# Performance work log

Measured on AMD Instinct MI355X. Metric: run time of the kernel, lower is better.

## Reference

```python
import jax, jax.numpy as jnp
import numpy as np

VOCAB, HDIM, NC = 32000, 256, 5
B, L = 256, 512  # L must be a power of 2 (complete binary tree, depth log2(L))


def setup_inputs() -> dict:
    key = jax.random.key(0)
    ks = jax.random.split(key, 8)
    s_e = 1.0 / np.sqrt(HDIM)
    s_r = 1.0 / np.sqrt(2 * HDIM)
    return {
        "tokens": jax.random.randint(ks[0], (B, L), 0, VOCAB),                        # leaf word ids
        "embed_table": jax.random.normal(ks[1], (VOCAB, HDIM), jnp.float32),          # nn.Embedding
        "WR_w": jax.random.uniform(ks[2], (HDIM, 2 * HDIM), jnp.float32, -s_r, s_r),  # Linear(2H->H)
        "WR_b": jax.random.uniform(ks[3], (HDIM,), jnp.float32, -s_r, s_r),
        "WF_w": jax.random.uniform(ks[4], (HDIM, HDIM), jnp.float32, -s_e, s_e),      # Linear(H->H)
        "WF_b": jax.random.uniform(ks[5], (HDIM,), jnp.float32, -s_e, s_e),
        "WO_w": jax.random.uniform(ks[6], (NC, HDIM), jnp.float32, -s_e, s_e),        # Linear(H->NC)
        "WO_b": jax.random.uniform(ks[7], (NC,), jnp.float32, -s_e, s_e),
    }


def reference(tokens, embed_table, WR_w, WR_b, WF_w, WF_b, WO_w, WO_b):
    # Leaves: embedding gather. [B, L, H]
    e = embed_table[tokens]
    # Batched-by-depth tree composition: tanh(WR(cat(left, right))) per level.
    # Loop is over log2(L) levels (static), fully vectorized within each level.
    while e.shape[1] > 1:
        cat = jnp.concatenate([e[:, 0::2], e[:, 1::2]], axis=-1)   # [B, n/2, 2H]
        e = jnp.tanh(jnp.einsum('bnd,hd->bnh', cat, WR_w) + WR_b)  # [B, n/2, H]
    root = e[:, 0]  # [B, H]
    # classify: WO(ReLU(WF(root)))
    hidden = jax.nn.relu(root @ WF_w.T + WF_b)
    return hidden @ WO_w.T + WO_b  # [B, NC] logits
```

## Files before the change

kernel.cpp:

```cpp
#include <hip/hip_runtime.h>
#include <hip/hip_bf16.h>

typedef __bf16 bf16_t;
typedef __bf16 bf16x8 __attribute__((ext_vector_type(8)));
typedef __bf16 bf16x4 __attribute__((ext_vector_type(4)));
typedef float f32x4 __attribute__((ext_vector_type(4)));

__device__ __forceinline__ bf16_t f2bf(float f) {
    __hip_bfloat16 h = __float2bfloat16(f);
    return __builtin_bit_cast(bf16_t, h);
}

__device__ __forceinline__ float tanh_fast(float s) {
    float e2x = __expf(2.0f * s);
    return 1.0f - 2.0f * __builtin_amdgcn_rcpf(e2x + 1.0f);
}

__device__ __forceinline__ int swz(int u) { return u ^ ((u >> 3) & 7); }
__device__ __forceinline__ int actswz(int a) {
    return a ^ ((((a >> 10) ^ (a >> 13)) & 7) << 4);
}

#define GLD16(g, l)                                                        \
    __builtin_amdgcn_global_load_lds(                                      \
        (const __attribute__((address_space(1))) void*)(g),                \
        (__attribute__((address_space(3))) void*)(l), 16, 0, 0)

#define WAITV3() asm volatile("s_waitcnt vmcnt(3)" ::: "memory")
#define WAITV2() asm volatile("s_waitcnt vmcnt(2)" ::: "memory")
#define WAITV0() asm volatile("s_waitcnt vmcnt(0)" ::: "memory")
#define BAR() __builtin_amdgcn_s_barrier()

__global__ void __launch_bounds__(256) setup_kernel(const float* __restrict__ table,
                                                    const float* __restrict__ WRw,
                                                    const float* __restrict__ WFw,
                                                    bf16_t* __restrict__ tableBf,
                                                    bf16_t* __restrict__ Wbf,
                                                    bf16_t* __restrict__ Wfrag,
                                                    float* __restrict__ WFwT) {
    const int b = blockIdx.x, tid = threadIdx.x;
    if (b < 8000) {
        int i = b * 256 + tid;
        float4 v = ((const float4*)table)[i];
        bf16x4 o;
        o[0] = f2bf(v.x); o[1] = f2bf(v.y); o[2] = f2bf(v.z); o[3] = f2bf(v.w);
        ((bf16x4*)tableBf)[i] = o;
    } else if (b < 8128) {
        int i = (b - 8000) * 256 + tid;
        float4 v = ((const float4*)WRw)[i];
        bf16x4 o;
        o[0] = f2bf(v.x); o[1] = f2bf(v.y); o[2] = f2bf(v.z); o[3] = f2bf(v.w);
        ((bf16x4*)Wbf)[i] = o;
    } else if (b < 8192) {
        int gt = (b - 8128) * 256 + tid;
        int n16 = gt >> 10, rem = gt & 1023;
        int kt = rem >> 6, ln = rem & 63;
        int r = n16 * 16 + (ln & 15);
        int c = kt * 32 + (ln >> 4) * 8;
        const float4* s = (const float4*)(WRw + (long)r * 512 + c);
        float4 v0 = s[0], v1 = s[1];
        bf16x8 o;
        o[0] = f2bf(v0.x); o[1] = f2bf(v0.y); o[2] = f2bf(v0.z); o[3] = f2bf(v0.w);
        o[4] = f2bf(v1.x); o[5] = f2bf(v1.y); o[6] = f2bf(v1.z); o[7] = f2bf(v1.w);
        *(bf16x8*)(Wfrag + (size_t)gt * 8) = o;
    } else {
        int i0 = (b - 8192) * 1024 + tid * 4;
        float4 v;
        v.x = WFw[((i0 + 0) & 255) * 256 + ((i0 + 0) >> 8)];
        v.y = WFw[((i0 + 1) & 255) * 256 + ((i0 + 1) >> 8)];
        v.z = WFw[((i0 + 2) & 255) * 256 + ((i0 + 2) >> 8)];
        v.w = WFw[((i0 + 3) & 255) * 256 + ((i0 + 3) >> 8)];
        *(float4*)(WFwT + i0) = v;
    }
}

__global__ void __launch_bounds__(512) l1_kernel(const int* __restrict__ tokens,
                                                 const bf16_t* __restrict__ tableBf,
                                                 const bf16_t* __restrict__ W,
                                                 const float* __restrict__ bias,
                                                 bf16_t* __restrict__ out) {
    __shared__ __align__(16) char lds[73728];
    const int tid = threadIdx.x, lane = tid & 63, w = tid >> 6;
    const int wm = w >> 2, wn = w & 3, lr = lane & 15, g = lane >> 4;
    const long brow = (long)blockIdx.x * 128;

    const int ua = (w << 6) + swz(lane);
    const int arow = ua >> 2, acolE = (ua & 3) << 3;
    const long m = brow + arow;
    const int tokA = tokens[2 * m], tokB = tokens[2 * m + 1];
    const bf16_t* paLo = tableBf + (long)tokA * 256 + acolE;
    const bf16_t* paHi = tableBf + (long)tokB * 256 + acolE;

    const int ub0 = (w << 6) + swz(lane);
    const int ub1 = ((w + 8) << 6) + swz(lane);
    const bf16_t* pb0 = W + (long)(ub0 >> 2) * 512 + ((ub0 & 3) << 3);
    const bf16_t* pb1 = W + (long)(ub1 >> 2) * 512 + ((ub1 & 3) << 3);

    float bv[4];
#pragma unroll
    for (int nt = 0; nt < 4; ++nt) bv[nt] = bias[(wn << 6) + (nt << 4) + lr];

    int offA[4], offB[4];
#pragma unroll
    for (int mt = 0; mt < 4; ++mt)
        offA[mt] = swz((((wm << 6) + (mt << 4) + lr) << 2) + g) << 4;
#pragma unroll
    for (int nt = 0; nt < 4; ++nt)
        offB[nt] = 8192 + (swz((((wn << 6) + (nt << 4) + lr) << 2) + g) << 4);

    auto stage = [&](int s, int kt) {
        char* base = lds + s * 24576;
        bool lo = kt < 256;
        GLD16((lo ? paLo : paHi) + (kt & 255), base + (w << 10));
        GLD16(pb0 + kt, base + 8192 + (w << 10));
        GLD16(pb1 + kt, base + 8192 + ((w + 8) << 10));
    };

    f32x4 acc[4][4];
    const f32x4 zero = {0.f, 0.f, 0.f, 0.f};
#pragma unroll
    for (int i = 0; i < 4; ++i)
#pragma unroll
        for (int j = 0; j < 4; ++j) acc[i][j] = zero;

    stage(0, 0);
    stage(1, 32);
    WAITV3(); BAR();

#pragma unroll
    for (int t = 0; t < 16; ++t) {
        const char* base = lds + (t % 3) * 24576;
        if (t + 2 < 16) stage((t + 2) % 3, (t + 2) << 5);
        bf16x8 af[4], bfr[4];
#pragma unroll
        for (int mt = 0; mt < 4; ++mt) af[mt] = *(const bf16x8*)(base + offA[mt]);
#pragma unroll
        for (int nt = 0; nt < 4; ++nt) bfr[nt] = *(const bf16x8*)(base + offB[nt]);
#pragma unroll
        for (int mt = 0; mt < 4; ++mt)
#pragma unroll
            for (int nt = 0; nt < 4; ++nt)
                acc[mt][nt] = __builtin_amdgcn_mfma_f32_16x16x32_bf16(
                    af[mt], bfr[nt], acc[mt][nt], 0, 0, 0);
        if (t < 14)      { WAITV3(); BAR(); }
        else if (t == 14){ WAITV0(); BAR(); }
    }

    const int crow = g << 2;
#pragma unroll
    for (int nt = 0; nt < 4; ++nt) {
        int col = (wn << 6) + (nt << 4) + lr;
#pragma unroll
        for (int mt = 0; mt < 4; ++mt) {
            long row0 = brow + (wm << 6) + (mt << 4) + crow;
#pragma unroll
            for (int r = 0; r < 4; ++r)
                out[(row0 + r) * 256 + col] = f2bf(tanh_fast(acc[mt][nt][r] + bv[nt]));
        }
    }
}

__global__ void __launch_bounds__(512) tree_kernel(const bf16_t* __restrict__ l1out,
                                                   const bf16_t* __restrict__ W,
                                                   const bf16_t* __restrict__ Wfrag,
                                                   const float* __restrict__ bias,
                                                   const float* __restrict__ WFwT,
                                                   const float* __restrict__ WFb,
                                                   const float* __restrict__ WOw,
                                                   const float* __restrict__ WOb,
                                                   float* __restrict__ out) {
    __shared__ __align__(16) char stg[73728];
    __shared__ __align__(16) char act[65536];
    __shared__ float hid[256];

    const int tid = threadIdx.x, lane = tid & 63, w = tid >> 6;
    const int wm = w >> 2, wn = w & 3, lr = lane & 15, g = lane >> 4;
    const int crow = g << 2;
    const bf16_t* Abase = l1out + (size_t)blockIdx.x * 65536;

    const int ua = (w << 6) + swz(lane);
    const bf16_t* pa = Abase + (long)(ua >> 2) * 512 + ((ua & 3) << 3);
    const int ub0 = (w << 6) + swz(lane);
    const int ub1 = ((w + 8) << 6) + swz(lane);
    const bf16_t* pb0 = W + (long)(ub0 >> 2) * 512 + ((ub0 & 3) << 3);
    const bf16_t* pb1 = W + (long)(ub1 >> 2) * 512 + ((ub1 & 3) << 3);

    float bv[4];
#pragma unroll
    for (int nt = 0; nt < 4; ++nt) bv[nt] = bias[(wn << 6) + (nt << 4) + lr];
    float bvT[2];
#pragma unroll
    for (int nt = 0; nt < 2; ++nt) bvT[nt] = bias[(w << 5) + (nt << 4) + lr];

    int offB[4];
#pragma unroll
    for (int nt = 0; nt < 4; ++nt)
        offB[nt] = swz((((wn << 6) + (nt << 4) + lr) << 2) + g) << 4;

    {
        int offA[4];
#pragma unroll
        for (int mt = 0; mt < 4; ++mt)
            offA[mt] = swz((((wm << 6) + (mt << 4) + lr) << 2) + g) << 4;

        auto stage = [&](int s, int kt) {
            char* base = stg + s * 24576;
            GLD16(pa + kt, base + (w << 10));
            GLD16(pb0 + kt, base + 8192 + (w << 10));
            GLD16(pb1 + kt, base + 8192 + ((w + 8) << 10));
        };

        f32x4 acc[4][4];
        const f32x4 zero = {0.f, 0.f, 0.f, 0.f};
#pragma unroll
        for (int i = 0; i < 4; ++i)
#pragma unroll
            for (int j = 0; j < 4; ++j) acc[i][j] = zero;

        stage(0, 0); stage(1, 32);
        WAITV3(); BAR();
#pragma unroll
        for (int t = 0; t < 16; ++t) {
            const char* base = stg + (t % 3) * 24576;
            if (t + 2 < 16) stage((t + 2) % 3, (t + 2) << 5);
            bf16x8 af[4], bfr[4];
#pragma unroll
            for (int mt = 0; mt < 4; ++mt) af[mt] = *(const bf16x8*)(base + 8192 * 0 + offA[mt]);
#pragma unroll
            for (int nt = 0; nt < 4; ++nt) bfr[nt] = *(const bf16x8*)(base + 8192 + offB[nt]);
#pragma unroll
            for (int mt = 0; mt < 4; ++mt)
#pragma unroll
                for (int nt = 0; nt < 4; ++nt)
                    acc[mt][nt] = __builtin_amdgcn_mfma_f32_16x16x32_bf16(
                        af[mt], bfr[nt], acc[mt][nt], 0, 0, 0);
            if (t < 14)      { WAITV3(); BAR(); }
            else if (t == 14){ WAITV0(); BAR(); }
        }
#pragma unroll
        for (int nt = 0; nt < 4; ++nt) {
            int col = (wn << 6) + (nt << 4) + lr;
#pragma unroll
            for (int mt = 0; mt < 4; ++mt) {
                int m0 = (wm << 6) + (mt << 4) + crow;
#pragma unroll
                for (int r = 0; r < 4; ++r) {
                    int a = ((m0 + r) << 9) + (col << 1);
                    *(bf16_t*)(act + actswz(a)) = f2bf(tanh_fast(acc[mt][nt][r] + bv[nt]));
                }
            }
        }
        __syncthreads();
    }

    {
        auto stageB = [&](int s, int kt) {
            char* base = stg + s * 16384;
            GLD16(pb0 + kt, base + (w << 10));
            GLD16(pb1 + kt, base + ((w + 8) << 10));
        };
        f32x4 acc[2][4];
        const f32x4 zero = {0.f, 0.f, 0.f, 0.f};
#pragma unroll
        for (int i = 0; i < 2; ++i)
#pragma unroll
            for (int j = 0; j < 4; ++j) acc[i][j] = zero;

        stageB(0, 0); stageB(1, 32);
        WAITV2(); BAR();
#pragma unroll
        for (int t = 0; t < 16; ++t) {
            const char* base = stg + (t % 3) * 16384;
            if (t + 2 < 16) stageB((t + 2) % 3, (t + 2) << 5);
            bf16x8 af[2], bfr[4];
#pragma unroll
            for (int mt = 0; mt < 2; ++mt) {
                int row = (wm << 5) + (mt << 4) + lr;
                int a = (row << 10) + (t << 6) + (g << 4);
                af[mt] = *(const bf16x8*)(act + actswz(a));
            }
#pragma unroll
            for (int nt = 0; nt < 4; ++nt) bfr[nt] = *(const bf16x8*)(base + offB[nt]);
#pragma unroll
            for (int mt = 0; mt < 2; ++mt)
#pragma unroll
                for (int nt = 0; nt < 4; ++nt)
                    acc[mt][nt] = __builtin_amdgcn_mfma_f32_16x16x32_bf16(
                        af[mt], bfr[nt], acc[mt][nt], 0, 0, 0);
            if (t < 14)      { WAITV2(); BAR(); }
            else if (t == 14){ WAITV0(); BAR(); }
        }
        __syncthreads();
#pragma unroll
        for (int nt = 0; nt < 4; ++nt) {
            int col = (wn << 6) + (nt << 4) + lr;
#pragma unroll
            for (int mt = 0; mt < 2; ++mt) {
                int m0 = (wm << 5) + (mt << 4) + crow;
#pragma unroll
                for (int r = 0; r < 4; ++r) {
                    int a = ((m0 + r) << 10) + (col << 1);
                    *(bf16_t*)(act + actswz(a)) = f2bf(tanh_fast(acc[mt][nt][r] + bv[nt]));
                }
            }
        }
        __syncthreads();
    }

    {
        auto stageB = [&](int s, int kt) {
            char* base = stg + s * 16384;
            GLD16(pb0 + kt, base + (w << 10));
            GLD16(pb1 + kt, base + ((w + 8) << 10));
        };
        f32x4 acc[4];
        const f32x4 zero = {0.f, 0.f, 0.f, 0.f};
#pragma unroll
        for (int j = 0; j < 4; ++j) acc[j] = zero;

        stageB(0, 0); stageB(1, 32);
        WAITV2(); BAR();
#pragma unroll
        for (int t = 0; t < 16; ++t) {
            const char* base = stg + (t % 3) * 16384;
            if (t + 2 < 16) stageB((t + 2) % 3, (t + 2) << 5);
            int row = (wm << 4) + lr;
            int a = (row << 11) + ((t >= 8) ? 1024 : 0) + ((t & 7) << 6) + (g << 4);
            bf16x8 af = *(const bf16x8*)(act + actswz(a));
            bf16x8 bfr[4];
#pragma unroll
            for (int nt = 0; nt < 4; ++nt) bfr[nt] = *(const bf16x8*)(base + offB[nt]);
#pragma unroll
            for (int nt = 0; nt < 4; ++nt)
                acc[nt] = __builtin_amdgcn_mfma_f32_16x16x32_bf16(af, bfr[nt], acc[nt], 0, 0, 0);
            if (t < 14)      { WAITV2(); BAR(); }
            else if (t == 14){ WAITV0(); BAR(); }
        }
        __syncthreads();
#pragma unroll
        for (int nt = 0; nt < 4; ++nt) {
            int col = (wn << 6) + (nt << 4) + lr;
#pragma unroll
            for (int r = 0; r < 4; ++r) {
                int m0 = (wm << 4) + crow + r;
                if (m0 < 32) {
                    int a = (m0 << 11) + (col << 1);
                    *(bf16_t*)(act + actswz(a)) = f2bf(tanh_fast(acc[nt][r] + bv[nt]));
                }
            }
        }
        __syncthreads();
    }

    {
        bf16x8 wreg[2][16];
#pragma unroll
        for (int nt = 0; nt < 2; ++nt)
#pragma unroll
            for (int kt = 0; kt < 16; ++kt)
                wreg[nt][kt] = *(const bf16x8*)(
                    Wfrag + (size_t)((((2 * w + nt) * 16 + kt) * 64 + lane)) * 8);

#pragma unroll
        for (int lev = 0; lev < 5; ++lev) {
            const int sA = 4096 << lev;
            const int half = sA >> 1;
            f32x4 acc[2];
            const f32x4 zero = {0.f, 0.f, 0.f, 0.f};
            acc[0] = zero; acc[1] = zero;
#pragma unroll
            for (int kt = 0; kt < 16; ++kt) {
                int a = (sA * lr + ((kt >= 8) ? half : 0) + ((kt & 7) << 6) + (g << 4)) & 65535;
                bf16x8 af = *(const bf16x8*)(act + actswz(a));
                acc[0] = __builtin_amdgcn_mfma_f32_16x16x32_bf16(af, wreg[0][kt], acc[0], 0, 0, 0);
                acc[1] = __builtin_amdgcn_mfma_f32_16x16x32_bf16(af, wreg[1][kt], acc[1], 0, 0, 0);
            }
            __syncthreads();
            const int valid = 16 >> lev;
#pragma unroll
            for (int nt = 0; nt < 2; ++nt) {
                int col = (w << 5) + (nt << 4) + lr;
#pragma unroll
                for (int r = 0; r < 4; ++r) {
                    int m0 = crow + r;
                    if (m0 < valid) {
                        int a = sA * m0 + (col << 1);
                        *(bf16_t*)(act + actswz(a)) = f2bf(tanh_fast(acc[nt][r] + bvT[nt]));
                    }
                }
            }
            __syncthreads();
        }
    }

    if (tid < 256) {
        const bf16_t* root = (const bf16_t*)act;
        float s = WFb[tid];
#pragma unroll 8
        for (int k = 0; k < 256; ++k)
            s += (float)root[k] * WFwT[k * 256 + tid];
        hid[tid] = fmaxf(s, 0.0f);
    }
    __syncthreads();

    if (w < 5) {
        const float* wo = WOw + w * 256;
        float p = hid[lane] * wo[lane] + hid[lane + 64] * wo[lane + 64] +
                  hid[lane + 128] * wo[lane + 128] + hid[lane + 192] * wo[lane + 192];
#pragma unroll
        for (int off = 32; off > 0; off >>= 1) p += __shfl_down(p, off);
        if (lane == 0) out[(long)blockIdx.x * 5 + w] = p + WOb[w];
    }
}

extern "C" void kernel_launch(void* const* d_in, const int* in_sizes, int n_in,
                              void* d_out, int out_size, void* d_ws, size_t ws_size,
                              hipStream_t stream) {
    const int*   tokens = (const int*)d_in[0];
    const float* table  = (const float*)d_in[1];
    const float* WRw    = (const float*)d_in[2];
    const float* WRb    = (const float*)d_in[3];
    const float* WFw    = (const float*)d_in[4];
    const float* WFb    = (const float*)d_in[5];
    const float* WOw    = (const float*)d_in[6];
    const float* WOb    = (const float*)d_in[7];
    float* out = (float*)d_out;

    char* ws = (char*)d_ws;
    bf16_t* tableBf = (bf16_t*)ws;
    bf16_t* Wbf   = (bf16_t*)(ws + (size_t)20971520);
    bf16_t* Wfrag = (bf16_t*)(ws + (size_t)22020096);
    float*  WFwT  = (float*)(ws + (size_t)23068672);
    bf16_t* l1out = (bf16_t*)(ws + (size_t)25165824);

    setup_kernel<<<8256, 256, 0, stream>>>(table, WRw, WFw, tableBf, Wbf, Wfrag, WFwT);
    l1_kernel<<<512, 512, 0, stream>>>(tokens, tableBf, Wbf, WRb, l1out);
    tree_kernel<<<256, 512, 0, stream>>>(l1out, Wbf, Wfrag, WRb, WFwT, WFb, WOw, WOb, out);
}
```

Baseline: 159.2 us.

## Fuse leaf layer into tree kernel with register-resident weight fragments

```diff
diff --git a/kernel.cpp b/kernel.cpp
--- a/kernel.cpp
+++ b/kernel.cpp
@@ -26,8 +26,7 @@
         (const __attribute__((address_space(1))) void*)(g),                \
         (__attribute__((address_space(3))) void*)(l), 16, 0, 0)
 
-#define WAITV3() asm volatile("s_waitcnt vmcnt(3)" ::: "memory")
-#define WAITV2() asm volatile("s_waitcnt vmcnt(2)" ::: "memory")
+#define WAITV1() asm volatile("s_waitcnt vmcnt(1)" ::: "memory")
 #define WAITV0() asm volatile("s_waitcnt vmcnt(0)" ::: "memory")
 #define BAR() __builtin_amdgcn_s_barrier()
 
@@ -35,7 +34,6 @@
                                                     const float* __restrict__ WRw,
                                                     const float* __restrict__ WFw,
                                                     bf16_t* __restrict__ tableBf,
-                                                    bf16_t* __restrict__ Wbf,
                                                     bf16_t* __restrict__ Wfrag,
                                                     float* __restrict__ WFwT) {
     const int b = blockIdx.x, tid = threadIdx.x;
@@ -45,14 +43,8 @@
         bf16x4 o;
         o[0] = f2bf(v.x); o[1] = f2bf(v.y); o[2] = f2bf(v.z); o[3] = f2bf(v.w);
         ((bf16x4*)tableBf)[i] = o;
-    } else if (b < 8128) {
-        int i = (b - 8000) * 256 + tid;
-        float4 v = ((const float4*)WRw)[i];
-        bf16x4 o;
-        o[0] = f2bf(v.x); o[1] = f2bf(v.y); o[2] = f2bf(v.z); o[3] = f2bf(v.w);
-        ((bf16x4*)Wbf)[i] = o;
-    } else if (b < 8192) {
-        int gt = (b - 8128) * 256 + tid;
+    } else if (b < 8064) {
+        int gt = (b - 8000) * 256 + tid;
         int n16 = gt >> 10, rem = gt & 1023;
         int kt = rem >> 6, ln = rem & 63;
         int r = n16 * 16 + (ln & 15);
@@ -64,7 +56,7 @@
         o[4] = f2bf(v1.x); o[5] = f2bf(v1.y); o[6] = f2bf(v1.z); o[7] = f2bf(v1.w);
         *(bf16x8*)(Wfrag + (size_t)gt * 8) = o;
     } else {
-        int i0 = (b - 8192) * 1024 + tid * 4;
+        int i0 = (b - 8064) * 1024 + tid * 4;
         float4 v;
         v.x = WFw[((i0 + 0) & 255) * 256 + ((i0 + 0) >> 8)];
         v.y = WFw[((i0 + 1) & 255) * 256 + ((i0 + 1) >> 8)];
@@ -74,323 +66,220 @@
     }
 }
 
-__global__ void __launch_bounds__(512) l1_kernel(const int* __restrict__ tokens,
-                                                 const bf16_t* __restrict__ tableBf,
-                                                 const bf16_t* __restrict__ W,
-                                                 const float* __restrict__ bias,
-                                                 bf16_t* __restrict__ out) {
-    __shared__ __align__(16) char lds[73728];
-    const int tid = threadIdx.x, lane = tid & 63, w = tid >> 6;
-    const int wm = w >> 2, wn = w & 3, lr = lane & 15, g = lane >> 4;
-    const long brow = (long)blockIdx.x * 128;
-
-    const int ua = (w << 6) + swz(lane);
-    const int arow = ua >> 2, acolE = (ua & 3) << 3;
-    const long m = brow + arow;
-    const int tokA = tokens[2 * m], tokB = tokens[2 * m + 1];
-    const bf16_t* paLo = tableBf + (long)tokA * 256 + acolE;
-    const bf16_t* paHi = tableBf + (long)tokB * 256 + acolE;
-
-    const int ub0 = (w << 6) + swz(lane);
-    const int ub1 = ((w + 8) << 6) + swz(lane);
-    const bf16_t* pb0 = W + (long)(ub0 >> 2) * 512 + ((ub0 & 3) << 3);
-    const bf16_t* pb1 = W + (long)(ub1 >> 2) * 512 + ((ub1 & 3) << 3);
-
-    float bv[4];
-#pragma unroll
-    for (int nt = 0; nt < 4; ++nt) bv[nt] = bias[(wn << 6) + (nt << 4) + lr];
-
-    int offA[4], offB[4];
-#pragma unroll
-    for (int mt = 0; mt < 4; ++mt)
-        offA[mt] = swz((((wm << 6) + (mt << 4) + lr) << 2) + g) << 4;
-#pragma unroll
-    for (int nt = 0; nt < 4; ++nt)
-        offB[nt] = 8192 + (swz((((wn << 6) + (nt << 4) + lr) << 2) + g) << 4);
-
-    auto stage = [&](int s, int kt) {
-        char* base = lds + s * 24576;
-        bool lo = kt < 256;
-        GLD16((lo ? paLo : paHi) + (kt & 255), base + (w << 10));
-        GLD16(pb0 + kt, base + 8192 + (w << 10));
-        GLD16(pb1 + kt, base + 8192 + ((w + 8) << 10));
-    };
-
-    f32x4 acc[4][4];
-    const f32x4 zero = {0.f, 0.f, 0.f, 0.f};
-#pragma unroll
-    for (int i = 0; i < 4; ++i)
-#pragma unroll
-        for (int j = 0; j < 4; ++j) acc[i][j] = zero;
-
-    stage(0, 0);
-    stage(1, 32);
-    WAITV3(); BAR();
-
-#pragma unroll
-    for (int t = 0; t < 16; ++t) {
-        const char* base = lds + (t % 3) * 24576;
-        if (t + 2 < 16) stage((t + 2) % 3, (t + 2) << 5);
-        bf16x8 af[4], bfr[4];
-#pragma unroll
-        for (int mt = 0; mt < 4; ++mt) af[mt] = *(const bf16x8*)(base + offA[mt]);
-#pragma unroll
-        for (int nt = 0; nt < 4; ++nt) bfr[nt] = *(const bf16x8*)(base + offB[nt]);
-#pragma unroll
-        for (int mt = 0; mt < 4; ++mt)
-#pragma unroll
-            for (int nt = 0; nt < 4; ++nt)
-                acc[mt][nt] = __builtin_amdgcn_mfma_f32_16x16x32_bf16(
-                    af[mt], bfr[nt], acc[mt][nt], 0, 0, 0);
-        if (t < 14)      { WAITV3(); BAR(); }
-        else if (t == 14){ WAITV0(); BAR(); }
-    }
-
-    const int crow = g << 2;
-#pragma unroll
-    for (int nt = 0; nt < 4; ++nt) {
-        int col = (wn << 6) + (nt << 4) + lr;
-#pragma unroll
-        for (int mt = 0; mt < 4; ++mt) {
-            long row0 = brow + (wm << 6) + (mt << 4) + crow;
-#pragma unroll
-            for (int r = 0; r < 4; ++r)
-                out[(row0 + r) * 256 + col] = f2bf(tanh_fast(acc[mt][nt][r] + bv[nt]));
-        }
-    }
-}
-
-__global__ void __launch_bounds__(512) tree_kernel(const bf16_t* __restrict__ l1out,
-                                                   const bf16_t* __restrict__ W,
-                                                   const bf16_t* __restrict__ Wfrag,
-                                                   const float* __restrict__ bias,
-                                                   const float* __restrict__ WFwT,
-                                                   const float* __restrict__ WFb,
-                                                   const float* __restrict__ WOw,
-                                                   const float* __restrict__ WOb,
-                                                   float* __restrict__ out) {
-    __shared__ __align__(16) char stg[73728];
+__global__ void __launch_bounds__(512, 2) fused_kernel(const int* __restrict__ tokens,
+                                                       const bf16_t* __restrict__ tableBf,
+                                                       const bf16_t* __restrict__ Wfrag,
+                                                       const float* __restrict__ bias,
+                                                       const float* __restrict__ WFwT,
+                                                       const float* __restrict__ WFb,
+                                                       const float* __restrict__ WOw,
+                                                       const float* __restrict__ WOb,
+                                                       float* __restrict__ out) {
+    __shared__ __align__(16) char stg[24576];
+    __shared__ __align__(16) char bufX[65536];
     __shared__ __align__(16) char act[65536];
     __shared__ float hid[256];
 
     const int tid = threadIdx.x, lane = tid & 63, w = tid >> 6;
-    const int wm = w >> 2, wn = w & 3, lr = lane & 15, g = lane >> 4;
-    const int crow = g << 2;
-    const bf16_t* Abase = l1out + (size_t)blockIdx.x * 65536;
-
-    const int ua = (w << 6) + swz(lane);
-    const bf16_t* pa = Abase + (long)(ua >> 2) * 512 + ((ua & 3) << 3);
-    const int ub0 = (w << 6) + swz(lane);
-    const int ub1 = ((w + 8) << 6) + swz(lane);
-    const bf16_t* pb0 = W + (long)(ub0 >> 2) * 512 + ((ub0 & 3) << 3);
-    const bf16_t* pb1 = W + (long)(ub1 >> 2) * 512 + ((ub1 & 3) << 3);
-
-    float bv[4];
-#pragma unroll
-    for (int nt = 0; nt < 4; ++nt) bv[nt] = bias[(wn << 6) + (nt << 4) + lr];
+    const int lr = lane & 15, g = lane >> 4, crow = g << 2;
+    const f32x4 zero = {0.f, 0.f, 0.f, 0.f};
+
     float bvT[2];
 #pragma unroll
     for (int nt = 0; nt < 2; ++nt) bvT[nt] = bias[(w << 5) + (nt << 4) + lr];
 
-    int offB[4];
-#pragma unroll
-    for (int nt = 0; nt < 4; ++nt)
-        offB[nt] = swz((((wn << 6) + (nt << 4) + lr) << 2) + g) << 4;
+    bf16x8 wreg[2][16];
+#pragma unroll
+    for (int nt = 0; nt < 2; ++nt)
+#pragma unroll
+        for (int kt = 0; kt < 16; ++kt)
+            wreg[nt][kt] = *(const bf16x8*)(
+                Wfrag + (size_t)((((w * 2 + nt) * 16 + kt) * 64 + lane)) * 8);
+
+    const int us = (w << 6) + swz(lane);
+    const int srow = us >> 2;
+    const int scolE = (us & 3) << 3;
+    char* dst = stg + (w << 10);
+    int offA1[8];
+#pragma unroll
+    for (int mt = 0; mt < 8; ++mt)
+        offA1[mt] = swz((((mt << 4) + lr) << 2) + g) << 4;
+
+#pragma unroll 1
+    for (int h = 0; h < 2; ++h) {
+        long mrow = (long)blockIdx.x * 256 + h * 128 + srow;
+        int tok0 = tokens[2 * mrow], tok1 = tokens[2 * mrow + 1];
+        const bf16_t* tLo = tableBf + (long)tok0 * 256 + scolE;
+        const bf16_t* tHi = tableBf + (long)tok1 * 256 + scolE;
+
+        auto stage = [&](int s, int kt) {
+            const bf16_t* src = (kt < 8) ? (tLo + (kt << 5)) : (tHi + ((kt - 8) << 5));
+            GLD16(src, dst + s * 8192);
+        };
+
+        f32x4 acc[8][2];
+#pragma unroll
+        for (int i = 0; i < 8; ++i) { acc[i][0] = zero; acc[i][1] = zero; }
+
+        stage(0, 0); stage(1, 1);
+        WAITV1(); BAR();
+#pragma unroll
+        for (int t = 0; t < 16; ++t) {
+            if (t + 2 < 16) stage((t + 2) % 3, t + 2);
+            const char* base = stg + (t % 3) * 8192;
+            bf16x8 af[8];
+#pragma unroll
+            for (int mt = 0; mt < 8; ++mt) af[mt] = *(const bf16x8*)(base + offA1[mt]);
+#pragma unroll
+            for (int mt = 0; mt < 8; ++mt)
+#pragma unroll
+                for (int nt = 0; nt < 2; ++nt)
+                    acc[mt][nt] = __builtin_amdgcn_mfma_f32_16x16x32_bf16(
+                        af[mt], wreg[nt][t], acc[mt][nt], 0, 0, 0);
+            if (t < 14)       { WAITV1(); BAR(); }
+            else if (t == 14) { WAITV0(); BAR(); }
+        }
+#pragma unroll
+        for (int nt = 0; nt < 2; ++nt) {
+            int col = (w << 5) + (nt << 4) + lr;
+#pragma unroll
+            for (int mt = 0; mt < 8; ++mt)
+#pragma unroll
+                for (int rr = 0; rr < 4; ++rr) {
+                    int r = (mt << 4) + crow + rr;
+                    int a = ((r >> 1) << 10) + ((r & 1) << 9) + (col << 1);
+                    *(bf16_t*)(bufX + actswz(a)) =
+                        f2bf(tanh_fast(acc[mt][nt][rr] + bvT[nt]));
+                }
+        }
+        __syncthreads();
+
+        f32x4 acc2[4][2];
+#pragma unroll
+        for (int i = 0; i < 4; ++i) { acc2[i][0] = zero; acc2[i][1] = zero; }
+#pragma unroll
+        for (int kt = 0; kt < 16; ++kt) {
+#pragma unroll
+            for (int mt = 0; mt < 4; ++mt) {
+                int a = (((mt << 4) + lr) << 10) + (kt << 6) + (g << 4);
+                bf16x8 af = *(const bf16x8*)(bufX + actswz(a));
+#pragma unroll
+                for (int nt = 0; nt < 2; ++nt)
+                    acc2[mt][nt] = __builtin_amdgcn_mfma_f32_16x16x32_bf16(
+                        af, wreg[nt][kt], acc2[mt][nt], 0, 0, 0);
+            }
+        }
+        __syncthreads();
+#pragma unroll
+        for (int nt = 0; nt < 2; ++nt) {
+            int col = (w << 5) + (nt << 4) + lr;
+#pragma unroll
+            for (int mt = 0; mt < 4; ++mt)
+#pragma unroll
+                for (int rr = 0; rr < 4; ++rr) {
+                    int q = (h << 6) + (mt << 4) + crow + rr;
+                    int a = (q << 9) + (col << 1);
+                    *(bf16_t*)(act + actswz(a)) =
+                        f2bf(tanh_fast(acc2[mt][nt][rr] + bvT[nt]));
+                }
+        }
+        __syncthreads();
+    }
 
     {
-        int offA[4];
-#pragma unroll
-        for (int mt = 0; mt < 4; ++mt)
-            offA[mt] = swz((((wm << 6) + (mt << 4) + lr) << 2) + g) << 4;
-
-        auto stage = [&](int s, int kt) {
-            char* base = stg + s * 24576;
-            GLD16(pa + kt, base + (w << 10));
-            GLD16(pb0 + kt, base + 8192 + (w << 10));
-            GLD16(pb1 + kt, base + 8192 + ((w + 8) << 10));
-        };
-
-        f32x4 acc[4][4];
-        const f32x4 zero = {0.f, 0.f, 0.f, 0.f};
-#pragma unroll
-        for (int i = 0; i < 4; ++i)
-#pragma unroll
-            for (int j = 0; j < 4; ++j) acc[i][j] = zero;
-
-        stage(0, 0); stage(1, 32);
-        WAITV3(); BAR();
-#pragma unroll
-        for (int t = 0; t < 16; ++t) {
-            const char* base = stg + (t % 3) * 24576;
-            if (t + 2 < 16) stage((t + 2) % 3, (t + 2) << 5);
-            bf16x8 af[4], bfr[4];
-#pragma unroll
-            for (int mt = 0; mt < 4; ++mt) af[mt] = *(const bf16x8*)(base + 8192 * 0 + offA[mt]);
-#pragma unroll
-            for (int nt = 0; nt < 4; ++nt) bfr[nt] = *(const bf16x8*)(base + 8192 + offB[nt]);
+        f32x4 acc[4][2];
+#pragma unroll
+        for (int i = 0; i < 4; ++i) { acc[i][0] = zero; acc[i][1] = zero; }
+#pragma unroll
+        for (int kt = 0; kt < 16; ++kt)
+#pragma unroll
+            for (int mt = 0; mt < 4; ++mt) {
+                int a = (((mt << 4) + lr) << 10) + (kt << 6) + (g << 4);
+                bf16x8 af = *(const bf16x8*)(act + actswz(a));
+#pragma unroll
+                for (int nt = 0; nt < 2; ++nt)
+                    acc[mt][nt] = __builtin_amdgcn_mfma_f32_16x16x32_bf16(
+                        af, wreg[nt][kt], acc[mt][nt], 0, 0, 0);
+            }
+        __syncthreads();
+#pragma unroll
+        for (int nt = 0; nt < 2; ++nt) {
+            int col = (w << 5) + (nt << 4) + lr;
 #pragma unroll
             for (int mt = 0; mt < 4; ++mt)
 #pragma unroll
-                for (int nt = 0; nt < 4; ++nt)
+                for (int rr = 0; rr < 4; ++rr) {
+                    int q = (mt << 4) + crow + rr;
+                    int a = (q << 10) + (col << 1);
+                    *(bf16_t*)(act + actswz(a)) =
+                        f2bf(tanh_fast(acc[mt][nt][rr] + bvT[nt]));
+                }
+        }
+        __syncthreads();
+    }
+
+    {
+        f32x4 acc[2][2];
+#pragma unroll
+        for (int i = 0; i < 2; ++i) { acc[i][0] = zero; acc[i][1] = zero; }
+#pragma unroll
+        for (int kt = 0; kt < 16; ++kt)
+#pragma unroll
+            for (int mt = 0; mt < 2; ++mt) {
+                int row = (mt << 4) + lr;
+                int a = (row << 11) + ((kt >= 8) ? 1024 : 0) + ((kt & 7) << 6) + (g << 4);
+                bf16x8 af = *(const bf16x8*)(act + actswz(a));
+#pragma unroll
+                for (int nt = 0; nt < 2; ++nt)
                     acc[mt][nt] = __builtin_amdgcn_mfma_f32_16x16x32_bf16(
-                        af[mt], bfr[nt], acc[mt][nt], 0, 0, 0);
-            if (t < 14)      { WAITV3(); BAR(); }
-            else if (t == 14){ WAITV0(); BAR(); }
-        }
-#pragma unroll
-        for (int nt = 0; nt < 4; ++nt) {
-            int col = (wn << 6) + (nt << 4) + lr;
-#pragma unroll
-            for (int mt = 0; mt < 4; ++mt) {
-                int m0 = (wm << 6) + (mt << 4) + crow;
-#pragma unroll
-                for (int r = 0; r < 4; ++r) {
-                    int a = ((m0 + r) << 9) + (col << 1);
-                    *(bf16_t*)(act + actswz(a)) = f2bf(tanh_fast(acc[mt][nt][r] + bv[nt]));
-                }
+                        af, wreg[nt][kt], acc[mt][nt], 0, 0, 0);
             }
-        }
-        __syncthreads();
-    }
-
-    {
-        auto stageB = [&](int s, int kt) {
-            char* base = stg + s * 16384;
-            GLD16(pb0 + kt, base + (w << 10));
-            GLD16(pb1 + kt, base + ((w + 8) << 10));
-        };
-        f32x4 acc[2][4];
-        const f32x4 zero = {0.f, 0.f, 0.f, 0.f};
-#pragma unroll
-        for (int i = 0; i < 2; ++i)
-#pragma unroll
-            for (int j = 0; j < 4; ++j) acc[i][j] = zero;
-
-        stageB(0, 0); stageB(1, 32);
-        WAITV2(); BAR();
-#pragma unroll
-        for (int t = 0; t < 16; ++t) {
-            const char* base = stg + (t % 3) * 16384;
-            if (t + 2 < 16) stageB((t + 2) % 3, (t + 2) << 5);
-            bf16x8 af[2], bfr[4];
-#pragma unroll
-            for (int mt = 0; mt < 2; ++mt) {
-                int row = (wm << 5) + (mt << 4) + lr;
-                int a = (row << 10) + (t << 6) + (g << 4);
-                af[mt] = *(const bf16x8*)(act + actswz(a));
+        __syncthreads();
+#pragma unroll
+        for (int nt = 0; nt < 2; ++nt) {
+            int col = (w << 5) + (nt << 4) + lr;
+#pragma unroll
+            for (int mt = 0; mt < 2; ++mt)
+#pragma unroll
+                for (int rr = 0; rr < 4; ++rr) {
+                    int q = (mt << 4) + crow + rr;
+                    int a = (q << 11) + (col << 1);
+                    *(bf16_t*)(act + actswz(a)) =
+                        f2bf(tanh_fast(acc[mt][nt][rr] + bvT[nt]));
+                }
+        }
+        __syncthreads();
+    }
+
+#pragma unroll 1
+    for (int lev = 0; lev < 5; ++lev) {
+        const int sA = 4096 << lev;
+        const int half_ = sA >> 1;
+        f32x4 acc[2];
+        acc[0] = zero; acc[1] = zero;
+#pragma unroll
+        for (int kt = 0; kt < 16; ++kt) {
+            int a = (sA * lr + ((kt >= 8) ? half_ : 0) + ((kt & 7) << 6) + (g << 4)) & 65535;
+            bf16x8 af = *(const bf16x8*)(act + actswz(a));
+            acc[0] = __builtin_amdgcn_mfma_f32_16x16x32_bf16(af, wreg[0][kt], acc[0], 0, 0, 0);
+            acc[1] = __builtin_amdgcn_mfma_f32_16x16x32_bf16(af, wreg[1][kt], acc[1], 0, 0, 0);
+        }
+        __syncthreads();
+        const int valid = 16 >> lev;
+#pragma unroll
+        for (int nt = 0; nt < 2; ++nt) {
+            int col = (w << 5) + (nt << 4) + lr;
+#pragma unroll
+            for (int rr = 0; rr < 4; ++rr) {
+                int m0 = crow + rr;
+                if (m0 < valid) {
+                    int a = sA * m0 + (col << 1);
+                    *(bf16_t*)(act + actswz(a)) =
+                        f2bf(tanh_fast(acc[nt][rr] + bvT[nt]));
+                }
             }
-#pragma unroll
-            for (int nt = 0; nt < 4; ++nt) bfr[nt] = *(const bf16x8*)(base + offB[nt]);
-#pragma unroll
-            for (int mt = 0; mt < 2; ++mt)
-#pragma unroll
-                for (int nt = 0; nt < 4; ++nt)
-                    acc[mt][nt] = __builtin_amdgcn_mfma_f32_16x16x32_bf16(
-                        af[mt], bfr[nt], acc[mt][nt], 0, 0, 0);
-            if (t < 14)      { WAITV2(); BAR(); }
-            else if (t == 14){ WAITV0(); BAR(); }
-        }
-        __syncthreads();
-#pragma unroll
-        for (int nt = 0; nt < 4; ++nt) {
-            int col = (wn << 6) + (nt << 4) + lr;
-#pragma unroll
-            for (int mt = 0; mt < 2; ++mt) {
-                int m0 = (wm << 5) + (mt << 4) + crow;
-#pragma unroll
-                for (int r = 0; r < 4; ++r) {
-                    int a = ((m0 + r) << 10) + (col << 1);
-                    *(bf16_t*)(act + actswz(a)) = f2bf(tanh_fast(acc[mt][nt][r] + bv[nt]));
-                }
-            }
-        }
-        __syncthreads();
-    }
-
-    {
-        auto stageB = [&](int s, int kt) {
-            char* base = stg + s * 16384;
-            GLD16(pb0 + kt, base + (w << 10));
-            GLD16(pb1 + kt, base + ((w + 8) << 10));
-        };
-        f32x4 acc[4];
-        const f32x4 zero = {0.f, 0.f, 0.f, 0.f};
-#pragma unroll
-        for (int j = 0; j < 4; ++j) acc[j] = zero;
-
-        stageB(0, 0); stageB(1, 32);
-        WAITV2(); BAR();
-#pragma unroll
-        for (int t = 0; t < 16; ++t) {
-            const char* base = stg + (t % 3) * 16384;
-            if (t + 2 < 16) stageB((t + 2) % 3, (t + 2) << 5);
-            int row = (wm << 4) + lr;
-            int a = (row << 11) + ((t >= 8) ? 1024 : 0) + ((t & 7) << 6) + (g << 4);
-            bf16x8 af = *(const bf16x8*)(act + actswz(a));
-            bf16x8 bfr[4];
-#pragma unroll
-            for (int nt = 0; nt < 4; ++nt) bfr[nt] = *(const bf16x8*)(base + offB[nt]);
-#pragma unroll
-            for (int nt = 0; nt < 4; ++nt)
-                acc[nt] = __builtin_amdgcn_mfma_f32_16x16x32_bf16(af, bfr[nt], acc[nt], 0, 0, 0);
-            if (t < 14)      { WAITV2(); BAR(); }
-            else if (t == 14){ WAITV0(); BAR(); }
-        }
-        __syncthreads();
-#pragma unroll
-        for (int nt = 0; nt < 4; ++nt) {
-            int col = (wn << 6) + (nt << 4) + lr;
-#pragma unroll
-            for (int r = 0; r < 4; ++r) {
-                int m0 = (wm << 4) + crow + r;
-                if (m0 < 32) {
-                    int a = (m0 << 11) + (col << 1);
-                    *(bf16_t*)(act + actswz(a)) = f2bf(tanh_fast(acc[nt][r] + bv[nt]));
-                }
-            }
-        }
-        __syncthreads();
-    }
-
-    {
-        bf16x8 wreg[2][16];
-#pragma unroll
-        for (int nt = 0; nt < 2; ++nt)
-#pragma unroll
-            for (int kt = 0; kt < 16; ++kt)
-                wreg[nt][kt] = *(const bf16x8*)(
-                    Wfrag + (size_t)((((2 * w + nt) * 16 + kt) * 64 + lane)) * 8);
-
-#pragma unroll
-        for (int lev = 0; lev < 5; ++lev) {
-            const int sA = 4096 << lev;
-            const int half = sA >> 1;
-            f32x4 acc[2];
-            const f32x4 zero = {0.f, 0.f, 0.f, 0.f};
-            acc[0] = zero; acc[1] = zero;
-#pragma unroll
-            for (int kt = 0; kt < 16; ++kt) {
-                int a = (sA * lr + ((kt >= 8) ? half : 0) + ((kt & 7) << 6) + (g << 4)) & 65535;
-                bf16x8 af = *(const bf16x8*)(act + actswz(a));
-                acc[0] = __builtin_amdgcn_mfma_f32_16x16x32_bf16(af, wreg[0][kt], acc[0], 0, 0, 0);
-                acc[1] = __builtin_amdgcn_mfma_f32_16x16x32_bf16(af, wreg[1][kt], acc[1], 0, 0, 0);
-            }
-            __syncthreads();
-            const int valid = 16 >> lev;
-#pragma unroll
-            for (int nt = 0; nt < 2; ++nt) {
-                int col = (w << 5) + (nt << 4) + lr;
-#pragma unroll
-                for (int r = 0; r < 4; ++r) {
-                    int m0 = crow + r;
-                    if (m0 < valid) {
-                        int a = sA * m0 + (col << 1);
-                        *(bf16_t*)(act + actswz(a)) = f2bf(tanh_fast(acc[nt][r] + bvT[nt]));
-                    }
-                }
-            }
-            __syncthreads();
-        }
+        }
+        __syncthreads();
     }
 
     if (tid < 256) {
@@ -428,12 +317,10 @@
 
     char* ws = (char*)d_ws;
     bf16_t* tableBf = (bf16_t*)ws;
-    bf16_t* Wbf   = (bf16_t*)(ws + (size_t)20971520);
-    bf16_t* Wfrag = (bf16_t*)(ws + (size_t)22020096);
-    float*  WFwT  = (float*)(ws + (size_t)23068672);
-    bf16_t* l1out = (bf16_t*)(ws + (size_t)25165824);
-
-    setup_kernel<<<8256, 256, 0, stream>>>(table, WRw, WFw, tableBf, Wbf, Wfrag, WFwT);
-    l1_kernel<<<512, 512, 0, stream>>>(tokens, tableBf, Wbf, WRb, l1out);
-    tree_kernel<<<256, 512, 0, stream>>>(l1out, Wbf, Wfrag, WRb, WFwT, WFb, WOw, WOb, out);
-}
+    bf16_t* Wfrag = (bf16_t*)(ws + (size_t)20971520);
+    float*  WFwT  = (float*)(ws + (size_t)22020096);
+
+    setup_kernel<<<8128, 256, 0, stream>>>(table, WRw, WFw, tableBf, Wfrag, WFwT);
+    fused_kernel<<<256, 512, 0, stream>>>(tokens, tableBf, Wfrag, WRb, WFwT,
+                                          WFb, WOw, WOb, out);
+}
```

Measured after the change: 225.8 us. 41.9% more time.
